# Kernel optimization log

Measured on AMD Instinct MI355X. Metric: run time of the kernel, lower is better.

## Reference

```python
import jax, jax.numpy as jnp
import numpy as np

B, S, C, H, RANK = 8, 1024, 1280, 8, 4
MERGE_SCALE = 1.0   # self.scale
LORA_SCALE = 1.0    # scale arg passed to __call__ (defaults 1.0)


def setup_inputs() -> dict:
    key = jax.random.key(0)
    ks = jax.random.split(key, 20)
    std = 1.0 / np.sqrt(C)
    rstd = 1.0 / np.sqrt(RANK)
    d = {
        "hidden_states": jax.random.normal(ks[0], (B, S, C), jnp.float32),
        "pose_feature": jax.random.normal(ks[1], (B, S, C), jnp.float32),
        # qkv_merge Linear (init to zeros in the module; use small random to exercise the path)
        "qkv_merge_w": jax.random.normal(ks[2], (C, C), jnp.float32) * (0.02 * std),
        "qkv_merge_b": jax.random.normal(ks[3], (C,), jnp.float32) * 0.01,
        # attn.to_q/k/v (bias-free, diffusers default) and to_out[0] (with bias). Stored [in, out].
        "wq": jax.random.normal(ks[4], (C, C), jnp.float32) * std,
        "wk": jax.random.normal(ks[5], (C, C), jnp.float32) * std,
        "wv": jax.random.normal(ks[6], (C, C), jnp.float32) * std,
        "wo": jax.random.normal(ks[7], (C, C), jnp.float32) * std,
        "bo": jax.random.normal(ks[8], (C,), jnp.float32) * 0.01,
        # LoRA layers: down [in, rank], up [rank, out] (up is zeros at init; random here)
        "q_lora_down": jax.random.normal(ks[9], (C, RANK), jnp.float32) * std,
        "q_lora_up": jax.random.normal(ks[10], (RANK, C), jnp.float32) * rstd,
        "k_lora_down": jax.random.normal(ks[11], (C, RANK), jnp.float32) * std,
        "k_lora_up": jax.random.normal(ks[12], (RANK, C), jnp.float32) * rstd,
        "v_lora_down": jax.random.normal(ks[13], (C, RANK), jnp.float32) * std,
        "v_lora_up": jax.random.normal(ks[14], (RANK, C), jnp.float32) * rstd,
        "out_lora_down": jax.random.normal(ks[15], (C, RANK), jnp.float32) * std,
        "out_lora_up": jax.random.normal(ks[16], (RANK, C), jnp.float32) * rstd,
        "num_heads": H,
    }
    return d


def _lora(x, down, up):
    # LoRALinearLayer with network_alpha=None -> scale factor 1
    return (x @ down) @ up


def reference(hidden_states, pose_feature, qkv_merge_w, qkv_merge_b,
              wq, wk, wv, wo, bo,
              q_lora_down, q_lora_up, k_lora_down, k_lora_up,
              v_lora_down, v_lora_up, out_lora_down, out_lora_up,
              num_heads):
    b, s, c = hidden_states.shape
    dh = c // num_heads
    # gated pose-merge (query_condition and key_value_condition -> shared qkv source)
    merged = (hidden_states + pose_feature) @ qkv_merge_w + qkv_merge_b
    x = merged * MERGE_SCALE + hidden_states  # [b, s, c]
    # LoRA-augmented projections
    q = x @ wq + LORA_SCALE * _lora(x, q_lora_down, q_lora_up)
    k = x @ wk + LORA_SCALE * _lora(x, k_lora_down, k_lora_up)
    v = x @ wv + LORA_SCALE * _lora(x, v_lora_down, v_lora_up)
    # head_to_batch_dim -> [b, h, s, dh]
    q = q.reshape(b, s, num_heads, dh).transpose(0, 2, 1, 3)
    k = k.reshape(b, s, num_heads, dh).transpose(0, 2, 1, 3)
    v = v.reshape(b, s, num_heads, dh).transpose(0, 2, 1, 3)
    # attn.get_attention_scores: baddbmm scaled by head_dim**-0.5, then softmax
    scores = jnp.einsum('bhqd,bhkd->bhqk', q, k) * (dh ** -0.5)
    probs = jax.nn.softmax(scores, axis=-1)
    out = jnp.einsum('bhqk,bhkd->bhqd', probs, v)
    # batch_to_head_dim -> [b, s, c]
    out = out.transpose(0, 2, 1, 3).reshape(b, s, c)
    # output projection + LoRA; to_out[1] is dropout (identity at eval)
    out = out @ wo + bo + LORA_SCALE * _lora(out, out_lora_down, out_lora_up)
    # residual_connection=False, rescale_output_factor=1.0
    return out
```

## Files before the change

kernel.cpp:

```cpp
#include <hip/hip_runtime.h>
#include <stdint.h>

typedef unsigned short u16;
typedef __attribute__((ext_vector_type(8))) short short8;
typedef __attribute__((ext_vector_type(4))) float f32x4;

__device__ __forceinline__ float b2f(u16 x){
  union { unsigned u; float f; } v; v.u = ((unsigned)x) << 16; return v.f;
}
__device__ __forceinline__ float b2fs(short x){ return b2f((u16)x); }
__device__ __forceinline__ u16 f2b(float f){
  union { float f; unsigned u; } v; v.f = f;
  unsigned u = v.u;
  u += 0x7FFFu + ((u >> 16) & 1u);
  return (u16)(u >> 16);
}
__device__ __forceinline__ float ldg_f(const void* p, int i, int f32){
  return f32 ? ((const float*)p)[i] : b2f(((const u16*)p)[i]);
}
__device__ __forceinline__ void gld16(const void* g, void* l){
  __builtin_amdgcn_global_load_lds(
      (__attribute__((address_space(1))) void*)(g),
      (__attribute__((address_space(3))) void*)(l), 16, 0, 0);
}

__global__ void detect_dtype(const u16* __restrict__ hid, int* __restrict__ flag){
  if (blockIdx.x == 0){
    int lane = threadIdx.x & 63;
    int plaus = 0;
    for (int i = lane; i < 512; i += 64){
      u16 v = hid[2 * i];
      int e = (v >> 7) & 0xFF;
      if ((e >= 100 && e <= 140) || (v & 0x7FFF) == 0) plaus++;
    }
    #pragma unroll
    for (int xm = 1; xm < 64; xm <<= 1) plaus += __shfl_xor(plaus, xm, 64);
    if (threadIdx.x == 0) *flag = (plaus < 400) ? 1 : 0;
  }
}

__global__ void make_t(const void* __restrict__ hid, const void* __restrict__ pose,
                       u16* __restrict__ t, const int* __restrict__ flag){
  int base = (blockIdx.x * 256 + threadIdx.x) * 8;
  short8 o;
  if (*flag){
    #pragma unroll
    for (int j = 0; j < 2; j++){
      float4 a = *(const float4*)((const float*)hid  + base + j * 4);
      float4 b = *(const float4*)((const float*)pose + base + j * 4);
      o[j * 4 + 0] = (short)f2b(a.x + b.x);
      o[j * 4 + 1] = (short)f2b(a.y + b.y);
      o[j * 4 + 2] = (short)f2b(a.z + b.z);
      o[j * 4 + 3] = (short)f2b(a.w + b.w);
    }
  } else {
    short8 a = *(const short8*)((const u16*)hid  + base);
    short8 b = *(const short8*)((const u16*)pose + base);
    #pragma unroll
    for (int j = 0; j < 8; j++) o[j] = (short)f2b(b2fs(a[j]) + b2fs(b[j]));
  }
  *(short8*)(t + base) = o;
}

__global__ void prep_w(const void* __restrict__ w, const void* __restrict__ dn,
                       const void* __restrict__ up, u16* __restrict__ WT,
                       int rowOff, float sc, const int* __restrict__ flag)
{
  __shared__ float tile[64][65];
  const int f = *flag;
  const int k0 = blockIdx.x * 64, n0 = blockIdx.y * 64;
  const int tr  = threadIdx.x >> 2;
  const int tc0 = (threadIdx.x & 3) * 16;
  #pragma unroll
  for (int i = 0; i < 16; i++)
    tile[tr][tc0 + i] = ldg_f(w, (k0 + tr) * 1280 + n0 + tc0 + i, f);
  __syncthreads();
  const int n = n0 + tr;
  float upv[4];
  if (dn){
    #pragma unroll
    for (int r = 0; r < 4; r++) upv[r] = ldg_f(up, r * 1280 + n, f);
  }
  u16 tmp[16];
  #pragma unroll
  for (int i = 0; i < 16; i++){
    int k = k0 + tc0 + i;
    float val = tile[tc0 + i][tr];
    if (dn){
      #pragma unroll
      for (int r = 0; r < 4; r++)
        val += ldg_f(dn, k * 4 + r, f) * upv[r];
    }
    tmp[i] = f2b(val * sc);
  }
  u16* dst = &WT[(rowOff + n) * 1280 + k0 + tc0];
  #pragma unroll
  for (int i = 0; i < 4; i++)
    *(ushort4*)(dst + i * 4) = *(ushort4*)(tmp + i * 4);
}

template<bool BIAS, bool RESID, bool RAWOUT, bool VSPLIT>
__global__ __launch_bounds__(256) void gemm_bt(
    const u16* __restrict__ A, const u16* __restrict__ BT,
    const void* __restrict__ bias, const void* __restrict__ resid,
    void* __restrict__ Cout, u16* __restrict__ vtg,
    int n0off, int NOUT, int Kdim, const int* __restrict__ flag)
{
  __shared__ alignas(16) u16 As[128 * 32];
  __shared__ alignas(16) u16 Bs[128 * 32];
  const int tid  = threadIdx.x;
  const int lane = tid & 63;
  const int w    = tid >> 6;
  const int wm   = w >> 1, wn = w & 1;
  const int quad = lane >> 4, l15 = lane & 15;
  const int tileM = blockIdx.y << 7;
  const int tileN = (blockIdx.x + n0off) << 7;
  const int f32 = (BIAS || RESID || RAWOUT) ? *flag : 0;

  f32x4 acc[4][4];
  #pragma unroll
  for (int mi = 0; mi < 4; mi++)
    #pragma unroll
    for (int ni = 0; ni < 4; ni++)
      acc[mi][ni] = (f32x4){0.f, 0.f, 0.f, 0.f};

  for (int k0 = 0; k0 < Kdim; k0 += 32){
    {
      int c = tid;
      gld16(&A [(tileM + (c >> 2)) * Kdim + k0 + ((c & 3) << 3)], (char*)As + c * 16);
      gld16(&BT[(tileN + (c >> 2)) * Kdim + k0 + ((c & 3) << 3)], (char*)Bs + c * 16);
      c = tid + 256;
      gld16(&A [(tileM + (c >> 2)) * Kdim + k0 + ((c & 3) << 3)], (char*)As + c * 16);
      gld16(&BT[(tileN + (c >> 2)) * Kdim + k0 + ((c & 3) << 3)], (char*)Bs + c * 16);
    }
    __syncthreads();

    short8 af[4], bfr[4];
    #pragma unroll
    for (int mi = 0; mi < 4; mi++)
      af[mi] = *(const short8*)(As + (wm * 64 + mi * 16 + l15) * 32 + quad * 8);
    #pragma unroll
    for (int ni = 0; ni < 4; ni++)
      bfr[ni] = *(const short8*)(Bs + (wn * 64 + ni * 16 + l15) * 32 + quad * 8);
    #pragma unroll
    for (int mi = 0; mi < 4; mi++)
      #pragma unroll
      for (int ni = 0; ni < 4; ni++)
        acc[mi][ni] = __builtin_amdgcn_mfma_f32_16x16x32_bf16(
            af[mi], bfr[ni], acc[mi][ni], 0, 0, 0);
    __syncthreads();
  }

  if (VSPLIT && tileN >= 2560){
    #pragma unroll
    for (int mi = 0; mi < 4; mi++){
      #pragma unroll
      for (int ni = 0; ni < 4; ni++){
        int col = tileN + wn * 64 + ni * 16 + l15;
        int hd = col - 2560;
        int hh = hd / 160;
        int dd = hd - hh * 160;
        int row0 = tileM + wm * 64 + mi * 16 + quad * 4;
        int bb = row0 >> 10;
        long addr = ((long)((bb * 8 + hh) * 160 + dd) << 10) | (long)(row0 & 1023);
        ushort4 pk;
        pk.x = f2b(acc[mi][ni][0]); pk.y = f2b(acc[mi][ni][1]);
        pk.z = f2b(acc[mi][ni][2]); pk.w = f2b(acc[mi][ni][3]);
        *(ushort4*)&vtg[addr] = pk;
      }
    }
  } else {
    #pragma unroll
    for (int mi = 0; mi < 4; mi++){
      #pragma unroll
      for (int ni = 0; ni < 4; ni++){
        int col = tileN + wn * 64 + ni * 16 + l15;
        float bv = 0.f;
        if (BIAS) bv = ldg_f(bias, col, f32);
        #pragma unroll
        for (int r = 0; r < 4; r++){
          int row = tileM + wm * 64 + mi * 16 + quad * 4 + r;
          float v = acc[mi][ni][r] + bv;
          if (RESID) v += ldg_f(resid, row * NOUT + col, f32);
          if (RAWOUT && f32) ((float*)Cout)[row * NOUT + col] = v;
          else               ((u16*)Cout)[row * NOUT + col]   = f2b(v);
        }
      }
    }
  }
}

__global__ __launch_bounds__(256, 2) void attn_mfma(
    const u16* __restrict__ qk, const u16* __restrict__ vtg,
    u16* __restrict__ out)
{
  __shared__ alignas(16) u16 Ks[2 * 64 * 160];
  __shared__ alignas(16) u16 Vt[160 * 64];
  __shared__ alignas(16) u16 Ps[4 * 32 * 72];

  const int tid  = threadIdx.x, lane = tid & 63, wv = tid >> 6;
  const int quad = lane >> 4,   l15  = lane & 15;
  const int bh = ((blockIdx.y >> 3) << 3) | blockIdx.x;
  const int qt = blockIdx.y & 7;
  const int b  = bh >> 3, h = bh & 7;
  const int rowBase = (b << 10) + (qt << 7);
  const int kBase   = b << 10;

  short8 qa[2][5];
  #pragma unroll
  for (int mi = 0; mi < 2; mi++)
    #pragma unroll
    for (int kk = 0; kk < 5; kk++)
      qa[mi][kk] = *(const short8*)&qk[
          (rowBase + wv * 32 + mi * 16 + l15) * 2560 + h * 160 + kk * 32 + quad * 8];

  f32x4 o[2][10];
  #pragma unroll
  for (int mi = 0; mi < 2; mi++)
    #pragma unroll
    for (int ni = 0; ni < 10; ni++)
      o[mi][ni] = (f32x4){0.f, 0.f, 0.f, 0.f};
  float mr[2][4], lr[2][4];
  #pragma unroll
  for (int mi = 0; mi < 2; mi++)
    #pragma unroll
    for (int r = 0; r < 4; r++){ mr[mi][r] = -1e30f; lr[mi][r] = 0.f; }

  #pragma unroll
  for (int i = 0; i < 5; i++){
    int c = tid + (i << 8);
    int kr = c / 20, kc = c % 20;
    gld16(&qk[(kBase + kr) * 2560 + 1280 + h * 160 + (kc << 3)],
          (char*)Ks + c * 16);
  }
  __syncthreads();

  int buf = 0;
  for (int kt = 0; kt < 16; kt++){
    #pragma unroll
    for (int i = 0; i < 5; i++){
      int c = tid + (i << 8);
      int d = c >> 3;
      int l = (c & 7) ^ (d & 7);
      gld16(&vtg[((bh * 160 + d) << 10) + (kt << 6) + (l << 3)],
            (char*)Vt + c * 16);
    }
    if (kt < 15){
      #pragma unroll
      for (int i = 0; i < 5; i++){
        int c = tid + (i << 8);
        int kr = c / 20, kc = c % 20;
        gld16(&qk[(kBase + ((kt + 1) << 6) + kr) * 2560 + 1280 + h * 160 + (kc << 3)],
              (char*)Ks + (buf ^ 1) * 20480 + c * 16);
      }
    }
    const u16* KsR = Ks + buf * 10240;

    f32x4 s[2][4];
    #pragma unroll
    for (int mi = 0; mi < 2; mi++)
      #pragma unroll
      for (int ni = 0; ni < 4; ni++)
        s[mi][ni] = (f32x4){0.f, 0.f, 0.f, 0.f};
    __builtin_amdgcn_s_setprio(1);
    #pragma unroll
    for (int kk = 0; kk < 5; kk++){
      #pragma unroll
      for (int ni = 0; ni < 4; ni++){
        short8 bf = *(const short8*)&KsR[(ni * 16 + l15) * 160 + kk * 32 + quad * 8];
        s[0][ni] = __builtin_amdgcn_mfma_f32_16x16x32_bf16(qa[0][kk], bf, s[0][ni], 0, 0, 0);
        s[1][ni] = __builtin_amdgcn_mfma_f32_16x16x32_bf16(qa[1][kk], bf, s[1][ni], 0, 0, 0);
      }
    }
    __builtin_amdgcn_s_setprio(0);

    float al[2][4];
    #pragma unroll
    for (int mi = 0; mi < 2; mi++){
      #pragma unroll
      for (int r = 0; r < 4; r++){
        float mx = fmaxf(fmaxf(s[mi][0][r], s[mi][1][r]),
                         fmaxf(s[mi][2][r], s[mi][3][r]));
        #pragma unroll
        for (int xm = 1; xm < 16; xm <<= 1) mx = fmaxf(mx, __shfl_xor(mx, xm, 64));
        float mn = fmaxf(mr[mi][r], mx);
        float a  = __expf(mr[mi][r] - mn);
        mr[mi][r] = mn; al[mi][r] = a;
        float sum = 0.f;
        #pragma unroll
        for (int ni = 0; ni < 4; ni++){
          float p = __expf(s[mi][ni][r] - mn);
          s[mi][ni][r] = p; sum += p;
        }
        #pragma unroll
        for (int xm = 1; xm < 16; xm <<= 1) sum += __shfl_xor(sum, xm, 64);
        lr[mi][r] = lr[mi][r] * a + sum;
      }
    }
    #pragma unroll
    for (int mi = 0; mi < 2; mi++)
      #pragma unroll
      for (int ni = 0; ni < 4; ni++)
        #pragma unroll
        for (int r = 0; r < 4; r++)
          Ps[wv * 2304 + (mi * 16 + quad * 4 + r) * 72 + ni * 16 + l15] =
              f2b(s[mi][ni][r]);
    #pragma unroll
    for (int mi = 0; mi < 2; mi++)
      #pragma unroll
      for (int ni = 0; ni < 10; ni++)
        #pragma unroll
        for (int r = 0; r < 4; r++)
          o[mi][ni][r] *= al[mi][r];

    if (kt < 15) asm volatile("s_waitcnt vmcnt(5)" ::: "memory");
    else         asm volatile("s_waitcnt vmcnt(0)" ::: "memory");
    __builtin_amdgcn_s_barrier();

    __builtin_amdgcn_s_setprio(1);
    #pragma unroll
    for (int kk2 = 0; kk2 < 2; kk2++){
      short8 pa0 = *(const short8*)&Ps[wv * 2304 + l15 * 72        + kk2 * 32 + quad * 8];
      short8 pa1 = *(const short8*)&Ps[wv * 2304 + (16 + l15) * 72 + kk2 * 32 + quad * 8];
      #pragma unroll
      for (int ni = 0; ni < 10; ni++){
        short8 vf = *(const short8*)&Vt[((ni * 16 + l15) << 6) +
                                        (((((kk2 << 2) | quad)) ^ (l15 & 7)) << 3)];
        o[0][ni] = __builtin_amdgcn_mfma_f32_16x16x32_bf16(pa0, vf, o[0][ni], 0, 0, 0);
        o[1][ni] = __builtin_amdgcn_mfma_f32_16x16x32_bf16(pa1, vf, o[1][ni], 0, 0, 0);
      }
    }
    __builtin_amdgcn_s_setprio(0);

    asm volatile("s_waitcnt vmcnt(0)" ::: "memory");
    __builtin_amdgcn_s_barrier();
    buf ^= 1;
  }

  #pragma unroll
  for (int mi = 0; mi < 2; mi++){
    #pragma unroll
    for (int r = 0; r < 4; r++){
      float inv = 1.0f / lr[mi][r];
      int row = rowBase + wv * 32 + mi * 16 + quad * 4 + r;
      #pragma unroll
      for (int ni = 0; ni < 10; ni++)
        out[row * 1280 + h * 160 + ni * 16 + l15] = f2b(o[mi][ni][r] * inv);
    }
  }
}

extern "C" void kernel_launch(void* const* d_in, const int* in_sizes, int n_in,
                              void* d_out, int out_size, void* d_ws, size_t ws_size,
                              hipStream_t stream)
{
  const void* hid  = d_in[0];
  const void* pose = d_in[1];
  const void* wm   = d_in[2];
  const void* mb   = d_in[3];
  const void* wq   = d_in[4];
  const void* wk   = d_in[5];
  const void* wv   = d_in[6];
  const void* wo   = d_in[7];
  const void* bo   = d_in[8];
  const void* qd   = d_in[9];
  const void* qu   = d_in[10];
  const void* kd   = d_in[11];
  const void* ku   = d_in[12];
  const void* vd   = d_in[13];
  const void* vu   = d_in[14];
  const void* od   = d_in[15];
  const void* ou   = d_in[16];
  (void)in_sizes; (void)n_in; (void)out_size; (void)ws_size;

  u16* ws   = (u16*)d_ws;
  u16* qk   = ws;
  u16* t    = qk;
  u16* x    = qk + 20971520;
  u16* vtg  = x + 10485760;
  u16* Wbuf = vtg + 10485760;
  u16* attnout = x;
  int* flag = (int*)(Wbuf + 4915200);

  const float qscale = 0.07905694150420949f;

  detect_dtype<<<1, 64, 0, stream>>>((const u16*)hid, flag);
  make_t<<<5120, 256, 0, stream>>>(hid, pose, t, flag);
  prep_w<<<dim3(20, 20), 256, 0, stream>>>(wm, nullptr, nullptr, Wbuf, 0, 1.0f, flag);
  gemm_bt<true, true, false, false><<<dim3(10, 64), 256, 0, stream>>>(
      t, Wbuf, mb, hid, x, nullptr, 0, 1280, 1280, flag);
  prep_w<<<dim3(20, 20), 256, 0, stream>>>(wq, qd, qu, Wbuf, 0, qscale, flag);
  prep_w<<<dim3(20, 20), 256, 0, stream>>>(wk, kd, ku, Wbuf, 1280, 1.0f, flag);
  prep_w<<<dim3(20, 20), 256, 0, stream>>>(wv, vd, vu, Wbuf, 2560, 1.0f, flag);
  gemm_bt<false, false, false, true><<<dim3(30, 64), 256, 0, stream>>>(
      x, Wbuf, nullptr, nullptr, qk, vtg, 0, 2560, 1280, flag);
  attn_mfma<<<dim3(8, 64), 256, 0, stream>>>(qk, vtg, attnout);
  prep_w<<<dim3(20, 20), 256, 0, stream>>>(wo, od, ou, Wbuf, 0, 1.0f, flag);
  gemm_bt<true, false, true, false><<<dim3(10, 64), 256, 0, stream>>>(
      attnout, Wbuf, bo, nullptr, d_out, nullptr, 0, 1280, 1280, flag);
}
```

Baseline: 539.5 us.

## Replace GEMM with 256x256 tile, double-buffered LDS pipeline and swizzled grid

Replaces the 128x128, 256-thread single-buffered GEMM with a 256x256-tile, 512-thread kernel using BK=64. LDS is double-buffered and the next tile's global-to-LDS loads are issued between MFMA phases, so memory latency overlaps compute. The kernel also XOR-swizzles LDS columns to avoid bank conflicts, raises MFMA wave priority, and remaps the 1D grid for L2 locality. The larger tiles mean far fewer blocks (160 for the 1280-wide GEMMs), which risks leaving CUs idle, and they raise register and LDS pressure per block.

```diff
diff --git a/kernel.cpp b/kernel.cpp
--- a/kernel.cpp
+++ b/kernel.cpp
@@ -99,68 +99,115 @@
     *(ushort4*)(dst + i * 4) = *(ushort4*)(tmp + i * 4);
 }
 
+#define GPHASE(KK, MH)                                                         \
+  {                                                                            \
+    if ((MH) == 0){                                                            \
+      _Pragma("unroll")                                                        \
+      for (int n = 0; n < 4; n++){                                             \
+        int R = wn * 64 + n * 16 + l15;                                        \
+        int c = (KK) * 32 + quad * 8;                                          \
+        bfr[n] = *(const short8*)&Bsm[b][R * 64 + (c ^ (((R >> 2) & 1) << 4))];\
+      }                                                                        \
+    }                                                                          \
+    short8 af[4];                                                              \
+    _Pragma("unroll")                                                          \
+    for (int j = 0; j < 4; j++){                                               \
+      int R = wm * 128 + ((MH) * 4 + j) * 16 + l15;                            \
+      int c = (KK) * 32 + quad * 8;                                            \
+      af[j] = *(const short8*)&Asm[b][R * 64 + (c ^ (((R >> 2) & 1) << 4))];   \
+    }                                                                          \
+    __builtin_amdgcn_s_barrier();                                              \
+    asm volatile("s_waitcnt lgkmcnt(0)" ::: "memory");                         \
+    __builtin_amdgcn_s_setprio(1);                                             \
+    _Pragma("unroll")                                                          \
+    for (int j = 0; j < 4; j++)                                                \
+      _Pragma("unroll")                                                        \
+      for (int n = 0; n < 4; n++)                                              \
+        acc[(MH) * 4 + j][n] = __builtin_amdgcn_mfma_f32_16x16x32_bf16(        \
+            af[j], bfr[n], acc[(MH) * 4 + j][n], 0, 0, 0);                     \
+    __builtin_amdgcn_s_setprio(0);                                             \
+    __builtin_amdgcn_s_barrier();                                              \
+  }
+
 template<bool BIAS, bool RESID, bool RAWOUT, bool VSPLIT>
-__global__ __launch_bounds__(256) void gemm_bt(
+__global__ __launch_bounds__(512, 2) void gemm256(
     const u16* __restrict__ A, const u16* __restrict__ BT,
     const void* __restrict__ bias, const void* __restrict__ resid,
     void* __restrict__ Cout, u16* __restrict__ vtg,
-    int n0off, int NOUT, int Kdim, const int* __restrict__ flag)
+    int gridX, int NOUT, int Kdim, const int* __restrict__ flag)
 {
-  __shared__ alignas(16) u16 As[128 * 32];
-  __shared__ alignas(16) u16 Bs[128 * 32];
+  __shared__ alignas(16) u16 Asm[2][256 * 64];
+  __shared__ alignas(16) u16 Bsm[2][256 * 64];
   const int tid  = threadIdx.x;
   const int lane = tid & 63;
   const int w    = tid >> 6;
-  const int wm   = w >> 1, wn = w & 1;
+  const int wm   = w >> 2, wn = w & 3;
   const int quad = lane >> 4, l15 = lane & 15;
-  const int tileM = blockIdx.y << 7;
-  const int tileN = (blockIdx.x + n0off) << 7;
+
+  const int nwg = gridDim.x;
+  const int id  = blockIdx.x;
+  const int swz = (id & 7) * (nwg >> 3) + (id >> 3);
+  const int bx  = swz % gridX;
+  const int by  = swz / gridX;
+  const int tileM = by << 8;
+  const int tileN = bx << 8;
   const int f32 = (BIAS || RESID || RAWOUT) ? *flag : 0;
 
-  f32x4 acc[4][4];
-  #pragma unroll
-  for (int mi = 0; mi < 4; mi++)
+  auto stageHalf = [&](int bufi, int half, int kt){
+    const int k0 = kt << 6;
+    #pragma unroll
+    for (int s = 0; s < 2; s++){
+      int cl  = s * 512 + tid;
+      int p   = ((half & 1) << 10) + cl;
+      int lc  = p ^ (((p >> 5) & 1) << 1);
+      int row = lc >> 3, slot = lc & 7;
+      if (half < 2)
+        gld16(&A [(tileM + row) * Kdim + k0 + slot * 8], (char*)Asm[bufi] + p * 16);
+      else
+        gld16(&BT[(tileN + row) * Kdim + k0 + slot * 8], (char*)Bsm[bufi] + p * 16);
+    }
+  };
+
+  f32x4 acc[8][4];
+  #pragma unroll
+  for (int mi = 0; mi < 8; mi++)
     #pragma unroll
     for (int ni = 0; ni < 4; ni++)
       acc[mi][ni] = (f32x4){0.f, 0.f, 0.f, 0.f};
 
-  for (int k0 = 0; k0 < Kdim; k0 += 32){
-    {
-      int c = tid;
-      gld16(&A [(tileM + (c >> 2)) * Kdim + k0 + ((c & 3) << 3)], (char*)As + c * 16);
-      gld16(&BT[(tileN + (c >> 2)) * Kdim + k0 + ((c & 3) << 3)], (char*)Bs + c * 16);
-      c = tid + 256;
-      gld16(&A [(tileM + (c >> 2)) * Kdim + k0 + ((c & 3) << 3)], (char*)As + c * 16);
-      gld16(&BT[(tileN + (c >> 2)) * Kdim + k0 + ((c & 3) << 3)], (char*)Bs + c * 16);
-    }
-    __syncthreads();
-
-    short8 af[4], bfr[4];
-    #pragma unroll
-    for (int mi = 0; mi < 4; mi++)
-      af[mi] = *(const short8*)(As + (wm * 64 + mi * 16 + l15) * 32 + quad * 8);
-    #pragma unroll
-    for (int ni = 0; ni < 4; ni++)
-      bfr[ni] = *(const short8*)(Bs + (wn * 64 + ni * 16 + l15) * 32 + quad * 8);
-    #pragma unroll
-    for (int mi = 0; mi < 4; mi++)
-      #pragma unroll
-      for (int ni = 0; ni < 4; ni++)
-        acc[mi][ni] = __builtin_amdgcn_mfma_f32_16x16x32_bf16(
-            af[mi], bfr[ni], acc[mi][ni], 0, 0, 0);
-    __syncthreads();
+  const int NT = Kdim >> 6;
+  stageHalf(0, 0, 0); stageHalf(0, 1, 0); stageHalf(0, 2, 0); stageHalf(0, 3, 0);
+  stageHalf(1, 0, 1); stageHalf(1, 1, 1);
+  asm volatile("s_waitcnt vmcnt(4)" ::: "memory");
+  __builtin_amdgcn_s_barrier();
+
+  for (int kt = 0; kt < NT; kt++){
+    const int b = kt & 1;
+    short8 bfr[4];
+    if (kt + 1 < NT) stageHalf(b ^ 1, 2, kt + 1);
+    GPHASE(0, 0)
+    if (kt + 1 < NT) stageHalf(b ^ 1, 3, kt + 1);
+    GPHASE(0, 1)
+    GPHASE(1, 0)
+    GPHASE(1, 1)
+    if (kt + 2 < NT){ stageHalf(b, 0, kt + 2); stageHalf(b, 1, kt + 2); }
+    if (kt + 1 < NT){
+      if (kt + 2 < NT) asm volatile("s_waitcnt vmcnt(4)" ::: "memory");
+      else             asm volatile("s_waitcnt vmcnt(0)" ::: "memory");
+      __builtin_amdgcn_s_barrier();
+    }
   }
 
   if (VSPLIT && tileN >= 2560){
     #pragma unroll
-    for (int mi = 0; mi < 4; mi++){
+    for (int mi = 0; mi < 8; mi++){
       #pragma unroll
       for (int ni = 0; ni < 4; ni++){
         int col = tileN + wn * 64 + ni * 16 + l15;
         int hd = col - 2560;
         int hh = hd / 160;
         int dd = hd - hh * 160;
-        int row0 = tileM + wm * 64 + mi * 16 + quad * 4;
+        int row0 = tileM + wm * 128 + mi * 16 + quad * 4;
         int bb = row0 >> 10;
         long addr = ((long)((bb * 8 + hh) * 160 + dd) << 10) | (long)(row0 & 1023);
         ushort4 pk;
@@ -171,7 +218,7 @@
     }
   } else {
     #pragma unroll
-    for (int mi = 0; mi < 4; mi++){
+    for (int mi = 0; mi < 8; mi++){
       #pragma unroll
       for (int ni = 0; ni < 4; ni++){
         int col = tileN + wn * 64 + ni * 16 + l15;
@@ -179,7 +226,7 @@
         if (BIAS) bv = ldg_f(bias, col, f32);
         #pragma unroll
         for (int r = 0; r < 4; r++){
-          int row = tileM + wm * 64 + mi * 16 + quad * 4 + r;
+          int row = tileM + wm * 128 + mi * 16 + quad * 4 + r;
           float v = acc[mi][ni][r] + bv;
           if (RESID) v += ldg_f(resid, row * NOUT + col, f32);
           if (RAWOUT && f32) ((float*)Cout)[row * NOUT + col] = v;
@@ -387,15 +434,15 @@
   detect_dtype<<<1, 64, 0, stream>>>((const u16*)hid, flag);
   make_t<<<5120, 256, 0, stream>>>(hid, pose, t, flag);
   prep_w<<<dim3(20, 20), 256, 0, stream>>>(wm, nullptr, nullptr, Wbuf, 0, 1.0f, flag);
-  gemm_bt<true, true, false, false><<<dim3(10, 64), 256, 0, stream>>>(
-      t, Wbuf, mb, hid, x, nullptr, 0, 1280, 1280, flag);
+  gemm256<true, true, false, false><<<160, 512, 0, stream>>>(
+      t, Wbuf, mb, hid, x, nullptr, 5, 1280, 1280, flag);
   prep_w<<<dim3(20, 20), 256, 0, stream>>>(wq, qd, qu, Wbuf, 0, qscale, flag);
   prep_w<<<dim3(20, 20), 256, 0, stream>>>(wk, kd, ku, Wbuf, 1280, 1.0f, flag);
   prep_w<<<dim3(20, 20), 256, 0, stream>>>(wv, vd, vu, Wbuf, 2560, 1.0f, flag);
-  gemm_bt<false, false, false, true><<<dim3(30, 64), 256, 0, stream>>>(
-      x, Wbuf, nullptr, nullptr, qk, vtg, 0, 2560, 1280, flag);
+  gemm256<false, false, false, true><<<480, 512, 0, stream>>>(
+      x, Wbuf, nullptr, nullptr, qk, vtg, 15, 2560, 1280, flag);
   attn_mfma<<<dim3(8, 64), 256, 0, stream>>>(qk, vtg, attnout);
   prep_w<<<dim3(20, 20), 256, 0, stream>>>(wo, od, ou, Wbuf, 0, 1.0f, flag);
-  gemm_bt<true, false, true, false><<<dim3(10, 64), 256, 0, stream>>>(
-      attnout, Wbuf, bo, nullptr, d_out, nullptr, 0, 1280, 1280, flag);
-}
+  gemm256<true, false, true, false><<<160, 512, 0, stream>>>(
+      attnout, Wbuf, bo, nullptr, d_out, nullptr, 5, 1280, 1280, flag);
+}
```

After: 577.0 us. 1.07x slower.
